# Performance work log

Hardware: AMD Instinct MI355X
Metric: run time of the kernel (lower is better)

The kernel has to match this reference:

```python
import jax, jax.numpy as jnp
import numpy as np
from jax import lax

CS = 64  # c_star


def _conv(x, w, pad, dil=1, groups=1):
    return lax.conv_general_dilated(
        x, w, (1, 1), ((pad[0], pad[0]), (pad[1], pad[1])),
        rhs_dilation=(dil, dil), dimension_numbers=('NCHW', 'OIHW', 'NCHW'),
        feature_group_count=groups)


def _bn(x, p, eps=1e-5):
    # p: [4, C] = (gamma, beta, running_mean, running_var), eval-mode batchnorm
    g, b, m, v = p
    s = g * lax.rsqrt(v + eps)
    return x * s[None, :, None, None] + (b - m * s)[None, :, None, None]


def _grid_sample(im, grid):
    # bilinear, padding_mode='zeros', align_corners=True
    # im: [B,C,H,W], grid: [B,H,W,2] with (x, y) in [-1, 1]
    B, C, H, W = im.shape
    gx = (grid[..., 0] + 1.0) * 0.5 * (W - 1)
    gy = (grid[..., 1] + 1.0) * 0.5 * (H - 1)
    x0 = jnp.floor(gx)
    y0 = jnp.floor(gy)
    wx = gx - x0
    wy = gy - y0

    def corner(ix, iy, w):
        valid = (ix >= 0) & (ix <= W - 1) & (iy >= 0) & (iy <= H - 1)
        ixc = jnp.clip(ix, 0, W - 1).astype(jnp.int32)
        iyc = jnp.clip(iy, 0, H - 1).astype(jnp.int32)
        vals = jax.vmap(lambda a, yy, xx: a[:, yy, xx])(im, iyc, ixc)  # [B,C,H,W]
        return vals * (w * valid)[:, None]

    return (corner(x0, y0, (1 - wx) * (1 - wy)) + corner(x0 + 1, y0, wx * (1 - wy))
            + corner(x0, y0 + 1, (1 - wx) * wy) + corner(x0 + 1, y0 + 1, wx * wy))


def _forward(x, w_reduce, bn_reduce, dcn_off_w, dcn_off_b, dcn_dw_w, dcn_pw_w, bn_dcn,
             w_d2, bn_d2, w_d3, bn_d3, w_asym1, bn_asym1, w_asym2, bn_asym2,
             ctx_weight, bn_star, eca_w, sp_w, blend_weight, w_expand, bn_expand):
    silu = jax.nn.silu
    h = silu(_bn(_conv(x, w_reduce, (0, 0)), bn_reduce))
    hs, hb = h[:, :CS], h[:, CS:]
    B, _, H, W = hs.shape
    # --- LightweightDCNv2 ---
    om = _conv(hs, dcn_off_w, (1, 1)) + dcn_off_b[None, :, None, None]
    off_y, off_x = om[:, 0], om[:, 1]
    mask = jax.nn.sigmoid(om[:, 2:3])
    gy, gx = jnp.meshgrid(jnp.linspace(-1.0, 1.0, H), jnp.linspace(-1.0, 1.0, W), indexing='ij')
    grid = jnp.stack([gx[None] + off_x * (2.0 / W), gy[None] + off_y * (2.0 / H)], axis=-1)
    xd = _grid_sample(hs, grid) * mask
    dcn = silu(_bn(_conv(_conv(xd, dcn_dw_w, (1, 1), groups=CS), dcn_pw_w, (0, 0)), bn_dcn))
    # --- context branches (depthwise dilated + asymmetric) ---
    d2 = silu(_bn(_conv(hs, w_d2, (2, 2), dil=2, groups=CS), bn_d2))
    d3 = silu(_bn(_conv(hs, w_d3, (3, 3), dil=3, groups=CS), bn_d3))
    a1 = silu(_bn(_conv(hs, w_asym1, (0, 3), groups=CS), bn_asym1))
    asym = silu(_bn(_conv(a1, w_asym2, (3, 0), groups=CS), bn_asym2))
    wv = jax.nn.softmax(ctx_weight)
    ctx = wv[0] * d2 + wv[1] * d3 + wv[2] * asym
    star = _bn(dcn * ctx, bn_star)
    # --- DualAttentionGate ---
    ych = star.mean((2, 3))[:, None, :]  # [B,1,C]
    ych = lax.conv_general_dilated(ych, eca_w, (1,), ((2, 2),),
                                   dimension_numbers=('NCH', 'OIH', 'NCH'))
    ych = jax.nn.sigmoid(ych).reshape(B, CS, 1, 1)
    star = star * ych
    sp = jnp.concatenate([star.mean(1, keepdims=True), star.max(1, keepdims=True)], axis=1)
    star = star * jax.nn.sigmoid(_conv(sp, sp_w, (3, 3)))
    # --- blend + shuffle + expand + residual ---
    alpha = jax.nn.sigmoid(blend_weight)
    out = jnp.concatenate([star * alpha, hb * (1.0 - alpha)], axis=1)
    c = out.shape[1]
    out = out.reshape(B, 2, c // 2, H, W).transpose(0, 2, 1, 3, 4).reshape(B, c, H, W)
    out = silu(_bn(_conv(out, w_expand, (0, 0)), bn_expand))
    return out + x


def setup_inputs() -> dict:
    ks = iter(jax.random.split(jax.random.key(0), 64))

    def nrm(shape, s=0.05):
        return jax.random.normal(next(ks), shape, jnp.float32) * s

    def bnp(C):
        return jnp.stack([1.0 + nrm((C,), 0.1), nrm((C,), 0.1), nrm((C,), 0.1),
                          0.5 + jax.random.uniform(next(ks), (C,), jnp.float32)])

    C1, C_, CSTAR = 256, 128, 64
    return dict(
        x=jax.random.normal(next(ks), (16, C1, 80, 80), jnp.float32),
        w_reduce=nrm((C_, C1, 1, 1)),
        bn_reduce=bnp(C_),
        dcn_off_w=nrm((3, CSTAR, 3, 3), 0.01),
        dcn_off_b=nrm((3,), 0.01),
        dcn_dw_w=nrm((CSTAR, 1, 3, 3), 0.2),
        dcn_pw_w=nrm((CSTAR, CSTAR, 1, 1), 0.1),
        bn_dcn=bnp(CSTAR),
        w_d2=nrm((CSTAR, 1, 3, 3), 0.2),
        bn_d2=bnp(CSTAR),
        w_d3=nrm((CSTAR, 1, 3, 3), 0.2),
        bn_d3=bnp(CSTAR),
        w_asym1=nrm((CSTAR, 1, 1, 7), 0.2),
        bn_asym1=bnp(CSTAR),
        w_asym2=nrm((CSTAR, 1, 7, 1), 0.2),
        bn_asym2=bnp(CSTAR),
        ctx_weight=jnp.ones(3, jnp.float32) / 3.0,
        bn_star=bnp(CSTAR),
        eca_w=nrm((1, 1, 5), 0.3),
        sp_w=nrm((1, 2, 7, 7), 0.1),
        blend_weight=jnp.asarray(0.5, jnp.float32),
        w_expand=nrm((C1, C_, 1, 1)),
        bn_expand=bnp(C1),
    )


def reference(x, w_reduce, bn_reduce, dcn_off_w, dcn_off_b, dcn_dw_w, dcn_pw_w, bn_dcn,
              w_d2, bn_d2, w_d3, bn_d3, w_asym1, bn_asym1, w_asym2, bn_asym2,
              ctx_weight, bn_star, eca_w, sp_w, blend_weight, w_expand, bn_expand):
    return _forward(x, w_reduce, bn_reduce, dcn_off_w, dcn_off_b, dcn_dw_w, dcn_pw_w, bn_dcn,
                    w_d2, bn_d2, w_d3, bn_d3, w_asym1, bn_asym1, w_asym2, bn_asym2,
                    ctx_weight, bn_star, eca_w, sp_w, blend_weight, w_expand, bn_expand)
```

## Files before the change

kernel.cpp:

```cpp
#include <hip/hip_runtime.h>

#define HH 80
#define WW 80
#define HWN 6400
#define BN 16

typedef unsigned short ushortT;
typedef __attribute__((ext_vector_type(8))) short short8;
typedef __attribute__((ext_vector_type(4))) float f32x4;

static constexpr size_t BIGN = (size_t)BN * 64 * HWN;

__device__ __forceinline__ float sigf(float v)  { return 1.f / (1.f + __expf(-v)); }
__device__ __forceinline__ float siluf(float v) { return v * sigf(v); }
__device__ __forceinline__ float tapf(const float* __restrict__ pl, int y, int x) {
  return ((unsigned)y < (unsigned)HH && (unsigned)x < (unsigned)WW) ? pl[y * WW + x] : 0.f;
}
__device__ __forceinline__ float bnap(float v, const float* __restrict__ bn, int c, int C) {
  float s = bn[c] * rsqrtf(bn[3 * C + c] + 1e-5f);
  return v * s + (bn[C + c] - bn[2 * C + c] * s);
}
__device__ __forceinline__ ushortT f2bf(float f) {
  unsigned u = __float_as_uint(f);
  return (ushortT)((u + 0x7FFFu + ((u >> 16) & 1u)) >> 16);
}
__device__ __forceinline__ void gl_lds16(const void* g, void* l) {
  __builtin_amdgcn_global_load_lds(
      (const __attribute__((address_space(1))) unsigned int*)g,
      (__attribute__((address_space(3))) unsigned int*)l, 16, 0, 0);
}
__device__ __forceinline__ int bs_w(int p, int k2) {
  return p * 20 + ((((k2 >> 2) ^ ((p >> 3) & 3)) << 2) | (k2 & 3));
}
__device__ __forceinline__ int bs_r(int p, int q) {
  return p * 20 + (((q ^ ((p >> 3) & 3)) << 2));
}

__global__ __launch_bounds__(256) void k_cvtw(const float* __restrict__ wr,
    const float* __restrict__ we, ushortT* __restrict__ wrb, ushortT* __restrict__ web) {
  int i = blockIdx.x * 256 + threadIdx.x;
  if (i < 32768) wrb[i] = f2bf(wr[i]);
  else           web[i - 32768] = f2bf(we[i - 32768]);
}

__global__ __launch_bounds__(256) void k_reduce_mfma(
    const float* __restrict__ x, const ushortT* __restrict__ Wb,
    const float* __restrict__ bn, float* __restrict__ hs, float* __restrict__ hb) {
  __shared__ ushortT As[128 * 32];
  __shared__ unsigned BsU[128 * 20];
  __shared__ float Ep[4 * 16 * 66];
  const int t = threadIdx.x;
  const int w = t >> 6, l = t & 63;
  const int p0 = blockIdx.x * 128;
  const int b = blockIdx.z;
  const int wm = (w >> 1) * 64, wn = (w & 1) * 64;
  f32x4 acc[4][4] = {};
  const float* xb = x + (size_t)b * 256 * HWN;
  const int srow = l >> 2, scol = (l & 3) * 8;
  for (int k0 = 0; k0 < 256; k0 += 32) {
    __syncthreads();
    gl_lds16(Wb + (size_t)((w * 2) * 16 + srow) * 256 + k0 + scol, &As[(w * 2) * 16 * 32]);
    gl_lds16(Wb + (size_t)((w * 2 + 1) * 16 + srow) * 256 + k0 + scol, &As[(w * 2 + 1) * 16 * 32]);
#pragma unroll
    for (int pass = 0; pass < 8; ++pass) {
      int idx = pass * 256 + t;
      int p_l = idx & 127, k2 = idx >> 7;
      int k = k0 + 2 * k2;
      float v0 = xb[(size_t)k * HWN + p0 + p_l];
      float v1 = xb[(size_t)(k + 1) * HWN + p0 + p_l];
      BsU[bs_w(p_l, k2)] = (unsigned)f2bf(v0) | ((unsigned)f2bf(v1) << 16);
    }
    __syncthreads();
    const int q = l >> 4, r16 = l & 15;
    short8 a[4], bv[4];
#pragma unroll
    for (int i = 0; i < 4; ++i)
      a[i] = *reinterpret_cast<const short8*>(&As[(wm + i * 16 + r16) * 32 + q * 8]);
#pragma unroll
    for (int j = 0; j < 4; ++j) {
      int row = wn + j * 16 + r16;
      bv[j] = *reinterpret_cast<const short8*>(&BsU[bs_r(row, q)]);
    }
#pragma unroll
    for (int i = 0; i < 4; ++i)
#pragma unroll
      for (int j = 0; j < 4; ++j)
        acc[i][j] = __builtin_amdgcn_mfma_f32_16x16x32_bf16(a[i], bv[j], acc[i][j], 0, 0, 0);
  }
  float* T = Ep + w * (16 * 66);
  const int col = l & 15, rowq = (l >> 4) * 4;
#pragma unroll
  for (int i = 0; i < 4; ++i) {
#pragma unroll
    for (int r = 0; r < 4; ++r)
#pragma unroll
      for (int j = 0; j < 4; ++j)
        T[(rowq + r) * 66 + j * 16 + col] = acc[i][j][r];
#pragma unroll
    for (int pass = 0; pass < 4; ++pass) {
      int row_l = pass * 4 + (l >> 4);
      const float4 v = *reinterpret_cast<const float4*>(&T[row_l * 66 + col * 4]);
      int c = wm + i * 16 + row_l;
      float s = bn[c] * rsqrtf(bn[384 + c] + 1e-5f);
      float tt = bn[128 + c] - bn[256 + c] * s;
      float4 o;
      o.x = siluf(v.x * s + tt);
      o.y = siluf(v.y * s + tt);
      o.z = siluf(v.z * s + tt);
      o.w = siluf(v.w * s + tt);
      float* dst = (c < 64 ? hs : hb) + ((size_t)b * 64 + (c & 63)) * HWN + p0 + wn + col * 4;
      *reinterpret_cast<float4*>(dst) = o;
    }
  }
}

__global__ __launch_bounds__(256) void k_offset(const float* __restrict__ hs,
    const float* __restrict__ w, const float* __restrict__ bias,
    float* __restrict__ sx, float* __restrict__ sy, float* __restrict__ msk) {
  __shared__ float tile[18 * 18];
  const int t = threadIdx.x;
  const int b = blockIdx.z;
  const int x0 = blockIdx.x * 16, y0 = blockIdx.y * 16;
  const int lx = t & 15, ly = t >> 4;
  float a0 = 0.f, a1 = 0.f, a2 = 0.f;
  for (int c = 0; c < 64; ++c) {
    __syncthreads();
    for (int i = t; i < 18 * 18; i += 256) {
      int tyy = i / 18, txx = i - tyy * 18;
      int gy = y0 + tyy - 1, gx = x0 + txx - 1;
      tile[i] = ((unsigned)gy < (unsigned)HH && (unsigned)gx < (unsigned)WW)
                    ? hs[((size_t)b * 64 + c) * HWN + gy * WW + gx] : 0.f;
    }
    __syncthreads();
    const float* wc = w + c * 9;
#pragma unroll
    for (int dy = 0; dy < 3; ++dy)
#pragma unroll
      for (int dx = 0; dx < 3; ++dx) {
        float v = tile[(ly + dy) * 18 + lx + dx];
        a0 = fmaf(wc[dy * 3 + dx], v, a0);
        a1 = fmaf(wc[576 + dy * 3 + dx], v, a1);
        a2 = fmaf(wc[1152 + dy * 3 + dx], v, a2);
      }
  }
  a0 += bias[0];
  a1 += bias[1];
  a2 += bias[2];
  size_t o = (size_t)b * HWN + (y0 + ly) * WW + x0 + lx;
  const float sc = 79.f / 80.f;
  sx[o] = (float)(x0 + lx) + a1 * sc;
  sy[o] = (float)(y0 + ly) + a0 * sc;
  msk[o] = sigf(a2);
}

__global__ __launch_bounds__(256) void k_gsdw(const float* __restrict__ hs,
    const float* __restrict__ sx, const float* __restrict__ sy,
    const float* __restrict__ msk, const float* __restrict__ wdw,
    float* __restrict__ outp) {
  __shared__ float tile[18 * 18];
  const int t = threadIdx.x;
  const int c = blockIdx.y, b = blockIdx.z;
  const int tx0 = (blockIdx.x % 5) * 16, ty0 = (blockIdx.x / 5) * 16;
  const float* pl = hs + ((size_t)b * 64 + c) * HWN;
  for (int i = t; i < 324; i += 256) {
    int iy = i / 18, ix = i - iy * 18;
    int gy = ty0 + iy - 1, gx = tx0 + ix - 1;
    float v = 0.f;
    if ((unsigned)gy < (unsigned)HH && (unsigned)gx < (unsigned)WW) {
      size_t o = (size_t)b * HWN + gy * WW + gx;
      float gxs = sx[o], gys = sy[o], m = msk[o];
      float x0f = floorf(gxs), y0f = floorf(gys);
      float wx = gxs - x0f, wy = gys - y0f;
      int ix0 = (int)x0f, iy0 = (int)y0f;
      int ix1 = ix0 + 1, iy1 = iy0 + 1;
      float acc = 0.f;
      if ((unsigned)iy0 < (unsigned)HH && (unsigned)ix0 < (unsigned)WW) acc = fmaf(pl[iy0 * WW + ix0], (1.f - wx) * (1.f - wy), acc);
      if ((unsigned)iy0 < (unsigned)HH && (unsigned)ix1 < (unsigned)WW) acc = fmaf(pl[iy0 * WW + ix1], wx * (1.f - wy), acc);
      if ((unsigned)iy1 < (unsigned)HH && (unsigned)ix0 < (unsigned)WW) acc = fmaf(pl[iy1 * WW + ix0], (1.f - wx) * wy, acc);
      if ((unsigned)iy1 < (unsigned)HH && (unsigned)ix1 < (unsigned)WW) acc = fmaf(pl[iy1 * WW + ix1], wx * wy, acc);
      v = acc * m;
    }
    tile[i] = v;
  }
  __syncthreads();
  const int lx = t & 15, ly = t >> 4;
  const float* wc = wdw + c * 9;
  float acc = 0.f;
#pragma unroll
  for (int dy = 0; dy < 3; ++dy)
#pragma unroll
    for (int dx = 0; dx < 3; ++dx)
      acc = fmaf(wc[dy * 3 + dx], tile[(ly + dy) * 18 + lx + dx], acc);
  outp[((size_t)b * 64 + c) * HWN + (ty0 + ly) * WW + tx0 + lx] = acc;
}

__global__ __launch_bounds__(256) void k_pw(const float* __restrict__ in,
    const float* __restrict__ w, const float* __restrict__ bn, float* __restrict__ outp) {
  __shared__ __align__(16) float Wt[1024];
  __shared__ __align__(16) float Xt[1024];
  const int t = threadIdx.x;
  const int p0 = blockIdx.x * 64, b = blockIdx.z;
  const int tx = t & 15, ty = t >> 4;
  float acc[4][4] = {};
  for (int k0 = 0; k0 < 64; k0 += 16) {
    __syncthreads();
    int idx = t;
#pragma unroll
    for (int r = 0; r < 4; ++r) {
      int c_l = idx >> 4, k_l = idx & 15;
      Wt[k_l * 64 + c_l] = w[c_l * 64 + k0 + k_l];
      idx += 256;
    }
    idx = t;
#pragma unroll
    for (int r = 0; r < 4; ++r) {
      int k_l = idx >> 6, p_l = idx & 63;
      Xt[k_l * 64 + p_l] = in[((size_t)b * 64 + k0 + k_l) * HWN + p0 + p_l];
      idx += 256;
    }
    __syncthreads();
#pragma unroll
    for (int kk = 0; kk < 16; ++kk) {
      const float4 wv = *reinterpret_cast<const float4*>(Wt + kk * 64 + ty * 4);
      const float4 xv = *reinterpret_cast<const float4*>(Xt + kk * 64 + tx * 4);
      const float wa[4] = {wv.x, wv.y, wv.z, wv.w};
      const float xa[4] = {xv.x, xv.y, xv.z, xv.w};
#pragma unroll
      for (int i = 0; i < 4; ++i)
#pragma unroll
        for (int j = 0; j < 4; ++j) acc[i][j] = fmaf(wa[i], xa[j], acc[i][j]);
    }
  }
#pragma unroll
  for (int i = 0; i < 4; ++i) {
    int c = ty * 4 + i;
    float s = bn[c] * rsqrtf(bn[192 + c] + 1e-5f);
    float tt = bn[64 + c] - bn[128 + c] * s;
    float4 o;
    o.x = siluf(acc[i][0] * s + tt);
    o.y = siluf(acc[i][1] * s + tt);
    o.z = siluf(acc[i][2] * s + tt);
    o.w = siluf(acc[i][3] * s + tt);
    *reinterpret_cast<float4*>(outp + ((size_t)b * 64 + c) * HWN + p0 + tx * 4) = o;
  }
}

__global__ __launch_bounds__(256) void k_ctxstar(const float* __restrict__ hs,
    const float* __restrict__ dcn,
    const float* __restrict__ wd2, const float* __restrict__ bnd2,
    const float* __restrict__ wd3, const float* __restrict__ bnd3,
    const float* __restrict__ wa1, const float* __restrict__ bna1,
    const float* __restrict__ wa2, const float* __restrict__ bna2,
    const float* __restrict__ cw, const float* __restrict__ bnstar,
    float* __restrict__ star0) {
  __shared__ float ht[22 * 23];
  __shared__ float at[22 * 17];
  const int t = threadIdx.x;
  const int c = blockIdx.y, b = blockIdx.z;
  const int tx0 = (blockIdx.x % 5) * 16, ty0 = (blockIdx.x / 5) * 16;
  const float* pl = hs + ((size_t)b * 64 + c) * HWN;
  for (int i = t; i < 484; i += 256) {
    int iy = i / 22, ix = i - iy * 22;
    int gy = ty0 + iy - 3, gx = tx0 + ix - 3;
    ht[iy * 23 + ix] = ((unsigned)gy < (unsigned)HH && (unsigned)gx < (unsigned)WW)
                           ? pl[gy * WW + gx] : 0.f;
  }
  __syncthreads();
  for (int i = t; i < 352; i += 256) {
    int iy = i >> 4, ix = i & 15;
    int gy = ty0 + iy - 3;
    float v = 0.f;
    if ((unsigned)gy < (unsigned)HH) {
      float s = 0.f;
#pragma unroll
      for (int k = 0; k < 7; ++k) s = fmaf(wa1[c * 7 + k], ht[iy * 23 + ix + k], s);
      v = siluf(bnap(s, bna1, c, 64));
    }
    at[iy * 17 + ix] = v;
  }
  __syncthreads();
  const int lx = t & 15, ly = t >> 4;
  float d2 = 0.f, d3 = 0.f;
#pragma unroll
  for (int dy = 0; dy < 3; ++dy)
#pragma unroll
    for (int dx = 0; dx < 3; ++dx) {
      float w2 = wd2[c * 9 + dy * 3 + dx], w3 = wd3[c * 9 + dy * 3 + dx];
      d2 = fmaf(w2, ht[(ly + 3 + 2 * (dy - 1)) * 23 + lx + 3 + 2 * (dx - 1)], d2);
      d3 = fmaf(w3, ht[(ly + 3 + 3 * (dy - 1)) * 23 + lx + 3 + 3 * (dx - 1)], d3);
    }
  float as = 0.f;
#pragma unroll
  for (int k = 0; k < 7; ++k) as = fmaf(wa2[c * 7 + k], at[(ly + k) * 17 + lx], as);
  d2 = siluf(bnap(d2, bnd2, c, 64));
  d3 = siluf(bnap(d3, bnd3, c, 64));
  as = siluf(bnap(as, bna2, c, 64));
  float e0 = __expf(cw[0]), e1 = __expf(cw[1]), e2 = __expf(cw[2]);
  float inv = 1.f / (e0 + e1 + e2);
  float ctx = (e0 * d2 + e1 * d3 + e2 * as) * inv;
  size_t o = ((size_t)b * 64 + c) * HWN + (ty0 + ly) * WW + tx0 + lx;
  star0[o] = bnap(dcn[o] * ctx, bnstar, c, 64);
}

__global__ __launch_bounds__(256) void k_cmean(const float* __restrict__ star0,
    float* __restrict__ mean) {
  const int c = blockIdx.x, b = blockIdx.y;
  const float* pl = star0 + ((size_t)b * 64 + c) * HWN;
  float s = 0.f;
  for (int i = threadIdx.x; i < HWN; i += 256) s += pl[i];
  __shared__ float red[256];
  red[threadIdx.x] = s;
  __syncthreads();
  for (int st = 128; st > 0; st >>= 1) {
    if (threadIdx.x < st) red[threadIdx.x] += red[threadIdx.x + st];
    __syncthreads();
  }
  if (threadIdx.x == 0) mean[b * 64 + c] = red[0] * (1.f / HWN);
}

__global__ __launch_bounds__(1024) void k_eca(const float* __restrict__ mean,
    const float* __restrict__ ew, float* __restrict__ ych) {
  const int t = threadIdx.x;
  const int c = t & 63;
  const int base = t - c;
  float acc = 0.f;
#pragma unroll
  for (int k = 0; k < 5; ++k) {
    int cc = c + k - 2;
    if ((unsigned)cc < 64u) acc = fmaf(ew[k], mean[base + cc], acc);
  }
  ych[t] = sigf(acc);
}

__global__ __launch_bounds__(256) void k_spstats(const float* __restrict__ star0,
    const float* __restrict__ ych, float* __restrict__ spmean, float* __restrict__ spmax) {
  __shared__ float yc[64];
  if (threadIdx.x < 64) yc[threadIdx.x] = ych[blockIdx.y * 64 + threadIdx.x];
  __syncthreads();
  const int p = blockIdx.x * 256 + threadIdx.x;
  const int b = blockIdx.y;
  float s = 0.f, mx = -1e30f;
  for (int c = 0; c < 64; ++c) {
    float v = star0[((size_t)b * 64 + c) * HWN + p] * yc[c];
    s += v;
    mx = fmaxf(mx, v);
  }
  spmean[(size_t)b * HWN + p] = s * (1.f / 64.f);
  spmax[(size_t)b * HWN + p] = mx;
}

__global__ __launch_bounds__(256) void k_spconv(const float* __restrict__ spmean,
    const float* __restrict__ spmax, const float* __restrict__ w,
    float* __restrict__ spat) {
  const int p = blockIdx.x * 256 + threadIdx.x;
  const int b = blockIdx.y;
  const int y = p / WW, x = p - y * WW;
  const float* me = spmean + (size_t)b * HWN;
  const float* mx = spmax + (size_t)b * HWN;
  float acc = 0.f;
#pragma unroll
  for (int dy = 0; dy < 7; ++dy) {
    int yy = y + dy - 3;
    if ((unsigned)yy >= (unsigned)HH) continue;
#pragma unroll
    for (int dx = 0; dx < 7; ++dx) {
      int xx = x + dx - 3;
      if ((unsigned)xx >= (unsigned)WW) continue;
      acc = fmaf(w[dy * 7 + dx], me[yy * WW + xx], acc);
      acc = fmaf(w[49 + dy * 7 + dx], mx[yy * WW + xx], acc);
    }
  }
  spat[(size_t)b * HWN + p] = sigf(acc);
}

__global__ __launch_bounds__(256) void k_expand_mfma(
    const float* __restrict__ star0, const float* __restrict__ hbuf,
    const float* __restrict__ ych, const float* __restrict__ spat,
    const float* __restrict__ blend, const ushortT* __restrict__ Wb,
    const float* __restrict__ bn, const float* __restrict__ xin,
    float* __restrict__ outp) {
  __shared__ ushortT As[128 * 32];
  __shared__ unsigned BsU[128 * 20];
  __shared__ float Ep[4 * 16 * 66];
  __shared__ float Sp[128];
  __shared__ float Yc[64];
  const int t = threadIdx.x;
  const int w = t >> 6, l = t & 63;
  const int p0 = blockIdx.x * 128;
  const int c0 = blockIdx.y * 128;
  const int b = blockIdx.z;
  const int wm = (w >> 1) * 64, wn = (w & 1) * 64;
  const float alpha = sigf(blend[0]);
  const float beta = 1.f - alpha;
  if (t < 128) Sp[t] = alpha * spat[(size_t)b * HWN + p0 + t];
  else if (t < 192) Yc[t - 128] = ych[b * 64 + (t - 128)];
  f32x4 acc[4][4] = {};
  const int srow = l >> 2, scol = (l & 3) * 8;
  for (int k0 = 0; k0 < 128; k0 += 32) {
    __syncthreads();
    gl_lds16(Wb + (size_t)(c0 + (w * 2) * 16 + srow) * 128 + k0 + scol, &As[(w * 2) * 16 * 32]);
    gl_lds16(Wb + (size_t)(c0 + (w * 2 + 1) * 16 + srow) * 128 + k0 + scol, &As[(w * 2 + 1) * 16 * 32]);
    const int ch0 = k0 >> 1;
#pragma unroll
    for (int pass = 0; pass < 8; ++pass) {
      int idx = pass * 256 + t;
      int p_l = idx & 127, chl = idx >> 7;
      int ch = ch0 + chl;
      size_t o = ((size_t)b * 64 + ch) * HWN + p0 + p_l;
      float vs = star0[o] * Yc[ch] * Sp[p_l];
      float vh = beta * hbuf[o];
      BsU[bs_w(p_l, chl)] = (unsigned)f2bf(vs) | ((unsigned)f2bf(vh) << 16);
    }
    __syncthreads();
    const int q = l >> 4, r16 = l & 15;
    short8 a[4], bv[4];
#pragma unroll
    for (int i = 0; i < 4; ++i)
      a[i] = *reinterpret_cast<const short8*>(&As[(wm + i * 16 + r16) * 32 + q * 8]);
#pragma unroll
    for (int j = 0; j < 4; ++j) {
      int row = wn + j * 16 + r16;
      bv[j] = *reinterpret_cast<const short8*>(&BsU[bs_r(row, q)]);
    }
#pragma unroll
    for (int i = 0; i < 4; ++i)
#pragma unroll
      for (int j = 0; j < 4; ++j)
        acc[i][j] = __builtin_amdgcn_mfma_f32_16x16x32_bf16(a[i], bv[j], acc[i][j], 0, 0, 0);
  }
  float* T = Ep + w * (16 * 66);
  const int col = l & 15, rowq = (l >> 4) * 4;
#pragma unroll
  for (int i = 0; i < 4; ++i) {
#pragma unroll
    for (int r = 0; r < 4; ++r)
#pragma unroll
      for (int j = 0; j < 4; ++j)
        T[(rowq + r) * 66 + j * 16 + col] = acc[i][j][r];
#pragma unroll
    for (int pass = 0; pass < 4; ++pass) {
      int row_l = pass * 4 + (l >> 4);
      const float4 v = *reinterpret_cast<const float4*>(&T[row_l * 66 + col * 4]);
      int c = c0 + wm + i * 16 + row_l;
      float s = bn[c] * rsqrtf(bn[768 + c] + 1e-5f);
      float tt = bn[256 + c] - bn[512 + c] * s;
      size_t o = ((size_t)b * 256 + c) * HWN + p0 + wn + col * 4;
      const float4 xr = *reinterpret_cast<const float4*>(xin + o);
      float4 ov;
      ov.x = siluf(v.x * s + tt) + xr.x;
      ov.y = siluf(v.y * s + tt) + xr.y;
      ov.z = siluf(v.z * s + tt) + xr.z;
      ov.w = siluf(v.w * s + tt) + xr.w;
      *reinterpret_cast<float4*>(outp + o) = ov;
    }
  }
}

extern "C" void kernel_launch(void* const* d_in, const int* in_sizes, int n_in,
                              void* d_out, int out_size, void* d_ws, size_t ws_size,
                              hipStream_t stream) {
  const float* x         = (const float*)d_in[0];
  const float* w_reduce  = (const float*)d_in[1];
  const float* bn_reduce = (const float*)d_in[2];
  const float* dcn_off_w = (const float*)d_in[3];
  const float* dcn_off_b = (const float*)d_in[4];
  const float* dcn_dw_w  = (const float*)d_in[5];
  const float* dcn_pw_w  = (const float*)d_in[6];
  const float* bn_dcn    = (const float*)d_in[7];
  const float* w_d2      = (const float*)d_in[8];
  const float* bn_d2     = (const float*)d_in[9];
  const float* w_d3      = (const float*)d_in[10];
  const float* bn_d3     = (const float*)d_in[11];
  const float* w_asym1   = (const float*)d_in[12];
  const float* bn_asym1  = (const float*)d_in[13];
  const float* w_asym2   = (const float*)d_in[14];
  const float* bn_asym2  = (const float*)d_in[15];
  const float* ctx_w     = (const float*)d_in[16];
  const float* bn_star   = (const float*)d_in[17];
  const float* eca_w     = (const float*)d_in[18];
  const float* sp_w      = (const float*)d_in[19];
  const float* blend     = (const float*)d_in[20];
  const float* w_expand  = (const float*)d_in[21];
  const float* bn_expand = (const float*)d_in[22];
  float* out = (float*)d_out;
  float* ws = (float*)d_ws;

  float* slotA = ws;
  float* slotB = ws + BIGN;
  float* slotC = ws + 2 * BIGN;
  float* slotD = ws + 3 * BIGN;
  float* sm = ws + 4 * BIGN;
  float* sx     = sm;
  float* sy     = sm + 102400;
  float* msk    = sm + 204800;
  float* spmean = sx;
  float* spmax  = sy;
  float* spat   = msk;
  float* cmean  = sm + 307200;
  float* ych    = sm + 308224;
  ushortT* Wrb = (ushortT*)(sm + 309248);
  ushortT* Web = Wrb + 32768;

  k_cvtw<<<dim3(256), 256, 0, stream>>>(w_reduce, w_expand, Wrb, Web);
  k_reduce_mfma<<<dim3(50, 1, 16), 256, 0, stream>>>(x, Wrb, bn_reduce, slotA, slotB);
  k_offset<<<dim3(5, 5, 16), 256, 0, stream>>>(slotA, dcn_off_w, dcn_off_b, sx, sy, msk);
  k_gsdw<<<dim3(25, 64, 16), 256, 0, stream>>>(slotA, sx, sy, msk, dcn_dw_w, slotC);
  k_pw<<<dim3(100, 1, 16), 256, 0, stream>>>(slotC, dcn_pw_w, bn_dcn, slotD);
  k_ctxstar<<<dim3(25, 64, 16), 256, 0, stream>>>(slotA, slotD, w_d2, bn_d2,
                                                  w_d3, bn_d3, w_asym1, bn_asym1,
                                                  w_asym2, bn_asym2, ctx_w, bn_star, slotD);
  k_cmean<<<dim3(64, 16), 256, 0, stream>>>(slotD, cmean);
  k_eca<<<dim3(1), 1024, 0, stream>>>(cmean, eca_w, ych);
  k_spstats<<<dim3(25, 16), 256, 0, stream>>>(slotD, ych, spmean, spmax);
  k_spconv<<<dim3(25, 16), 256, 0, stream>>>(spmean, spmax, sp_w, spat);
  k_expand_mfma<<<dim3(50, 2, 16), 256, 0, stream>>>(slotD, slotB, ych, spat, blend,
                                                     Web, bn_expand, x, out);
}
```

Baseline: 518.3 us.

## Port pointwise conv to bf16 MFMA and retune offset, spstats, epilogue padding

```diff
diff --git a/kernel.cpp b/kernel.cpp
--- a/kernel.cpp
+++ b/kernel.cpp
@@ -13,9 +13,6 @@
 
 __device__ __forceinline__ float sigf(float v)  { return 1.f / (1.f + __expf(-v)); }
 __device__ __forceinline__ float siluf(float v) { return v * sigf(v); }
-__device__ __forceinline__ float tapf(const float* __restrict__ pl, int y, int x) {
-  return ((unsigned)y < (unsigned)HH && (unsigned)x < (unsigned)WW) ? pl[y * WW + x] : 0.f;
-}
 __device__ __forceinline__ float bnap(float v, const float* __restrict__ bn, int c, int C) {
   float s = bn[c] * rsqrtf(bn[3 * C + c] + 1e-5f);
   return v * s + (bn[C + c] - bn[2 * C + c] * s);
@@ -37,10 +34,12 @@
 }
 
 __global__ __launch_bounds__(256) void k_cvtw(const float* __restrict__ wr,
-    const float* __restrict__ we, ushortT* __restrict__ wrb, ushortT* __restrict__ web) {
+    const float* __restrict__ we, const float* __restrict__ wp,
+    ushortT* __restrict__ wrb, ushortT* __restrict__ web, ushortT* __restrict__ wpb) {
   int i = blockIdx.x * 256 + threadIdx.x;
   if (i < 32768) wrb[i] = f2bf(wr[i]);
-  else           web[i - 32768] = f2bf(we[i - 32768]);
+  else if (i < 65536) web[i - 32768] = f2bf(we[i - 32768]);
+  else if (i < 69632) wpb[i - 65536] = f2bf(wp[i - 65536]);
 }
 
 __global__ __launch_bounds__(256) void k_reduce_mfma(
@@ -48,7 +47,7 @@
     const float* __restrict__ bn, float* __restrict__ hs, float* __restrict__ hb) {
   __shared__ ushortT As[128 * 32];
   __shared__ unsigned BsU[128 * 20];
-  __shared__ float Ep[4 * 16 * 66];
+  __shared__ float Ep[4 * 16 * 68];
   const int t = threadIdx.x;
   const int w = t >> 6, l = t & 63;
   const int p0 = blockIdx.x * 128;
@@ -87,7 +86,7 @@
       for (int j = 0; j < 4; ++j)
         acc[i][j] = __builtin_amdgcn_mfma_f32_16x16x32_bf16(a[i], bv[j], acc[i][j], 0, 0, 0);
   }
-  float* T = Ep + w * (16 * 66);
+  float* T = Ep + w * (16 * 68);
   const int col = l & 15, rowq = (l >> 4) * 4;
 #pragma unroll
   for (int i = 0; i < 4; ++i) {
@@ -95,11 +94,11 @@
     for (int r = 0; r < 4; ++r)
 #pragma unroll
       for (int j = 0; j < 4; ++j)
-        T[(rowq + r) * 66 + j * 16 + col] = acc[i][j][r];
+        T[(rowq + r) * 68 + j * 16 + col] = acc[i][j][r];
 #pragma unroll
     for (int pass = 0; pass < 4; ++pass) {
       int row_l = pass * 4 + (l >> 4);
-      const float4 v = *reinterpret_cast<const float4*>(&T[row_l * 66 + col * 4]);
+      const float4 v = *reinterpret_cast<const float4*>(&T[row_l * 68 + col * 4]);
       int c = wm + i * 16 + row_l;
       float s = bn[c] * rsqrtf(bn[384 + c] + 1e-5f);
       float tt = bn[128 + c] - bn[256 + c] * s;
@@ -117,31 +116,37 @@
 __global__ __launch_bounds__(256) void k_offset(const float* __restrict__ hs,
     const float* __restrict__ w, const float* __restrict__ bias,
     float* __restrict__ sx, float* __restrict__ sy, float* __restrict__ msk) {
-  __shared__ float tile[18 * 18];
-  const int t = threadIdx.x;
-  const int b = blockIdx.z;
-  const int x0 = blockIdx.x * 16, y0 = blockIdx.y * 16;
+  __shared__ float ht[16 * 324];
+  __shared__ float wt[1728];
+  const int t = threadIdx.x;
+  const int b = blockIdx.y;
+  const int x0 = (blockIdx.x % 5) * 16, y0 = (blockIdx.x / 5) * 16;
   const int lx = t & 15, ly = t >> 4;
+  for (int i = t; i < 1728; i += 256) wt[i] = w[i];
   float a0 = 0.f, a1 = 0.f, a2 = 0.f;
-  for (int c = 0; c < 64; ++c) {
-    __syncthreads();
-    for (int i = t; i < 18 * 18; i += 256) {
-      int tyy = i / 18, txx = i - tyy * 18;
-      int gy = y0 + tyy - 1, gx = x0 + txx - 1;
-      tile[i] = ((unsigned)gy < (unsigned)HH && (unsigned)gx < (unsigned)WW)
-                    ? hs[((size_t)b * 64 + c) * HWN + gy * WW + gx] : 0.f;
-    }
-    __syncthreads();
-    const float* wc = w + c * 9;
-#pragma unroll
-    for (int dy = 0; dy < 3; ++dy)
-#pragma unroll
-      for (int dx = 0; dx < 3; ++dx) {
-        float v = tile[(ly + dy) * 18 + lx + dx];
-        a0 = fmaf(wc[dy * 3 + dx], v, a0);
-        a1 = fmaf(wc[576 + dy * 3 + dx], v, a1);
-        a2 = fmaf(wc[1152 + dy * 3 + dx], v, a2);
-      }
+  for (int r = 0; r < 4; ++r) {
+    __syncthreads();
+    for (int i = t; i < 16 * 324; i += 256) {
+      int ch = i / 324, pos = i - ch * 324;
+      int iy = pos / 18, ix = pos - iy * 18;
+      int gy = y0 + iy - 1, gx = x0 + ix - 1;
+      ht[i] = ((unsigned)gy < (unsigned)HH && (unsigned)gx < (unsigned)WW)
+                  ? hs[((size_t)b * 64 + r * 16 + ch) * HWN + gy * WW + gx] : 0.f;
+    }
+    __syncthreads();
+    for (int ch = 0; ch < 16; ++ch) {
+      const float* base = &ht[ch * 324];
+      const int c = r * 16 + ch;
+#pragma unroll
+      for (int dy = 0; dy < 3; ++dy)
+#pragma unroll
+        for (int dx = 0; dx < 3; ++dx) {
+          float v = base[(ly + dy) * 18 + lx + dx];
+          a0 = fmaf(wt[c * 9 + dy * 3 + dx], v, a0);
+          a1 = fmaf(wt[576 + c * 9 + dy * 3 + dx], v, a1);
+          a2 = fmaf(wt[1152 + c * 9 + dy * 3 + dx], v, a2);
+        }
+    }
   }
   a0 += bias[0];
   a1 += bias[1];
@@ -194,54 +199,72 @@
   outp[((size_t)b * 64 + c) * HWN + (ty0 + ly) * WW + tx0 + lx] = acc;
 }
 
-__global__ __launch_bounds__(256) void k_pw(const float* __restrict__ in,
-    const float* __restrict__ w, const float* __restrict__ bn, float* __restrict__ outp) {
-  __shared__ __align__(16) float Wt[1024];
-  __shared__ __align__(16) float Xt[1024];
-  const int t = threadIdx.x;
-  const int p0 = blockIdx.x * 64, b = blockIdx.z;
-  const int tx = t & 15, ty = t >> 4;
-  float acc[4][4] = {};
-  for (int k0 = 0; k0 < 64; k0 += 16) {
-    __syncthreads();
-    int idx = t;
-#pragma unroll
-    for (int r = 0; r < 4; ++r) {
-      int c_l = idx >> 4, k_l = idx & 15;
-      Wt[k_l * 64 + c_l] = w[c_l * 64 + k0 + k_l];
-      idx += 256;
-    }
-    idx = t;
-#pragma unroll
-    for (int r = 0; r < 4; ++r) {
-      int k_l = idx >> 6, p_l = idx & 63;
-      Xt[k_l * 64 + p_l] = in[((size_t)b * 64 + k0 + k_l) * HWN + p0 + p_l];
-      idx += 256;
-    }
-    __syncthreads();
-#pragma unroll
-    for (int kk = 0; kk < 16; ++kk) {
-      const float4 wv = *reinterpret_cast<const float4*>(Wt + kk * 64 + ty * 4);
-      const float4 xv = *reinterpret_cast<const float4*>(Xt + kk * 64 + tx * 4);
-      const float wa[4] = {wv.x, wv.y, wv.z, wv.w};
-      const float xa[4] = {xv.x, xv.y, xv.z, xv.w};
-#pragma unroll
-      for (int i = 0; i < 4; ++i)
-#pragma unroll
-        for (int j = 0; j < 4; ++j) acc[i][j] = fmaf(wa[i], xa[j], acc[i][j]);
-    }
-  }
+__global__ __launch_bounds__(256) void k_pw_mfma(const float* __restrict__ in,
+    const ushortT* __restrict__ Wpb, const float* __restrict__ bn,
+    float* __restrict__ outp) {
+  __shared__ ushortT As[2][64 * 32];
+  __shared__ unsigned BsU[128 * 20];
+  __shared__ float Ep[4 * 16 * 36];
+  const int t = threadIdx.x;
+  const int w = t >> 6, l = t & 63;
+  const int p0 = blockIdx.x * 128;
+  const int b = blockIdx.y;
+  const int wn = w * 32;
+  f32x4 acc[4][2] = {};
+  const int srow = l >> 2, scol = (l & 3) * 8;
+  gl_lds16(Wpb + (size_t)(w * 16 + srow) * 64 + scol,      &As[0][w * 16 * 32]);
+  gl_lds16(Wpb + (size_t)(w * 16 + srow) * 64 + 32 + scol, &As[1][w * 16 * 32]);
+  for (int kc = 0; kc < 2; ++kc) {
+    __syncthreads();
+    const int ch0 = kc * 32;
+#pragma unroll
+    for (int pass = 0; pass < 8; ++pass) {
+      int idx = pass * 256 + t;
+      int p_l = idx & 127, k2 = idx >> 7;
+      int k = ch0 + 2 * k2;
+      float v0 = in[((size_t)b * 64 + k) * HWN + p0 + p_l];
+      float v1 = in[((size_t)b * 64 + k + 1) * HWN + p0 + p_l];
+      BsU[bs_w(p_l, k2)] = (unsigned)f2bf(v0) | ((unsigned)f2bf(v1) << 16);
+    }
+    __syncthreads();
+    const int q = l >> 4, r16 = l & 15;
+    short8 a[4], bv[2];
+#pragma unroll
+    for (int i = 0; i < 4; ++i)
+      a[i] = *reinterpret_cast<const short8*>(&As[kc][(i * 16 + r16) * 32 + q * 8]);
+#pragma unroll
+    for (int j = 0; j < 2; ++j)
+      bv[j] = *reinterpret_cast<const short8*>(&BsU[bs_r(wn + j * 16 + r16, q)]);
+#pragma unroll
+    for (int i = 0; i < 4; ++i)
+#pragma unroll
+      for (int j = 0; j < 2; ++j)
+        acc[i][j] = __builtin_amdgcn_mfma_f32_16x16x32_bf16(a[i], bv[j], acc[i][j], 0, 0, 0);
+  }
+  float* T = Ep + w * (16 * 36);
+  const int col = l & 15, rowq = (l >> 4) * 4;
 #pragma unroll
   for (int i = 0; i < 4; ++i) {
-    int c = ty * 4 + i;
-    float s = bn[c] * rsqrtf(bn[192 + c] + 1e-5f);
-    float tt = bn[64 + c] - bn[128 + c] * s;
-    float4 o;
-    o.x = siluf(acc[i][0] * s + tt);
-    o.y = siluf(acc[i][1] * s + tt);
-    o.z = siluf(acc[i][2] * s + tt);
-    o.w = siluf(acc[i][3] * s + tt);
-    *reinterpret_cast<float4*>(outp + ((size_t)b * 64 + c) * HWN + p0 + tx * 4) = o;
+#pragma unroll
+    for (int r = 0; r < 4; ++r)
+#pragma unroll
+      for (int j = 0; j < 2; ++j)
+        T[(rowq + r) * 36 + j * 16 + col] = acc[i][j][r];
+#pragma unroll
+    for (int pass = 0; pass < 2; ++pass) {
+      int flat = pass * 64 + l;
+      int row_l = flat >> 3, c4 = flat & 7;
+      const float4 v = *reinterpret_cast<const float4*>(&T[row_l * 36 + c4 * 4]);
+      int c = i * 16 + row_l;
+      float s = bn[c] * rsqrtf(bn[192 + c] + 1e-5f);
+      float tt = bn[64 + c] - bn[128 + c] * s;
+      float4 o;
+      o.x = siluf(v.x * s + tt);
+      o.y = siluf(v.y * s + tt);
+      o.z = siluf(v.z * s + tt);
+      o.w = siluf(v.w * s + tt);
+      *reinterpret_cast<float4*>(outp + ((size_t)b * 64 + c) * HWN + p0 + wn + c4 * 4) = o;
+    }
   }
 }
 
@@ -335,18 +358,29 @@
 __global__ __launch_bounds__(256) void k_spstats(const float* __restrict__ star0,
     const float* __restrict__ ych, float* __restrict__ spmean, float* __restrict__ spmax) {
   __shared__ float yc[64];
-  if (threadIdx.x < 64) yc[threadIdx.x] = ych[blockIdx.y * 64 + threadIdx.x];
+  __shared__ float rs[4][64], rm[4][64];
+  const int t = threadIdx.x;
+  const int b = blockIdx.y;
+  const int p0 = blockIdx.x * 64;
+  if (t < 64) yc[t] = ych[b * 64 + t];
   __syncthreads();
-  const int p = blockIdx.x * 256 + threadIdx.x;
-  const int b = blockIdx.y;
+  const int tq = t >> 6, pix = t & 63;
   float s = 0.f, mx = -1e30f;
-  for (int c = 0; c < 64; ++c) {
-    float v = star0[((size_t)b * 64 + c) * HWN + p] * yc[c];
+  for (int cc = 0; cc < 16; ++cc) {
+    int c = tq * 16 + cc;
+    float v = star0[((size_t)b * 64 + c) * HWN + p0 + pix] * yc[c];
     s += v;
     mx = fmaxf(mx, v);
   }
-  spmean[(size_t)b * HWN + p] = s * (1.f / 64.f);
-  spmax[(size_t)b * HWN + p] = mx;
+  rs[tq][pix] = s;
+  rm[tq][pix] = mx;
+  __syncthreads();
+  if (t < 64) {
+    float ss = rs[0][t] + rs[1][t] + rs[2][t] + rs[3][t];
+    float mm = fmaxf(fmaxf(rm[0][t], rm[1][t]), fmaxf(rm[2][t], rm[3][t]));
+    spmean[(size_t)b * HWN + p0 + t] = ss * (1.f / 64.f);
+    spmax[(size_t)b * HWN + p0 + t] = mm;
+  }
 }
 
 __global__ __launch_bounds__(256) void k_spconv(const float* __restrict__ spmean,
@@ -381,7 +415,7 @@
     float* __restrict__ outp) {
   __shared__ ushortT As[128 * 32];
   __shared__ unsigned BsU[128 * 20];
-  __shared__ float Ep[4 * 16 * 66];
+  __shared__ float Ep[4 * 16 * 68];
   __shared__ float Sp[128];
   __shared__ float Yc[64];
   const int t = threadIdx.x;
@@ -428,7 +462,7 @@
       for (int j = 0; j < 4; ++j)
         acc[i][j] = __builtin_amdgcn_mfma_f32_16x16x32_bf16(a[i], bv[j], acc[i][j], 0, 0, 0);
   }
-  float* T = Ep + w * (16 * 66);
+  float* T = Ep + w * (16 * 68);
   const int col = l & 15, rowq = (l >> 4) * 4;
 #pragma unroll
   for (int i = 0; i < 4; ++i) {
@@ -436,11 +470,11 @@
     for (int r = 0; r < 4; ++r)
 #pragma unroll
       for (int j = 0; j < 4; ++j)
-        T[(rowq + r) * 66 + j * 16 + col] = acc[i][j][r];
+        T[(rowq + r) * 68 + j * 16 + col] = acc[i][j][r];
 #pragma unroll
     for (int pass = 0; pass < 4; ++pass) {
       int row_l = pass * 4 + (l >> 4);
-      const float4 v = *reinterpret_cast<const float4*>(&T[row_l * 66 + col * 4]);
+      const float4 v = *reinterpret_cast<const float4*>(&T[row_l * 68 + col * 4]);
       int c = c0 + wm + i * 16 + row_l;
       float s = bn[c] * rsqrtf(bn[768 + c] + 1e-5f);
       float tt = bn[256 + c] - bn[512 + c] * s;
@@ -500,18 +534,19 @@
   float* ych    = sm + 308224;
   ushortT* Wrb = (ushortT*)(sm + 309248);
   ushortT* Web = Wrb + 32768;
-
-  k_cvtw<<<dim3(256), 256, 0, stream>>>(w_reduce, w_expand, Wrb, Web);
+  ushortT* Wpb = Web + 32768;
+
+  k_cvtw<<<dim3(272), 256, 0, stream>>>(w_reduce, w_expand, dcn_pw_w, Wrb, Web, Wpb);
   k_reduce_mfma<<<dim3(50, 1, 16), 256, 0, stream>>>(x, Wrb, bn_reduce, slotA, slotB);
-  k_offset<<<dim3(5, 5, 16), 256, 0, stream>>>(slotA, dcn_off_w, dcn_off_b, sx, sy, msk);
+  k_offset<<<dim3(25, 16), 256, 0, stream>>>(slotA, dcn_off_w, dcn_off_b, sx, sy, msk);
   k_gsdw<<<dim3(25, 64, 16), 256, 0, stream>>>(slotA, sx, sy, msk, dcn_dw_w, slotC);
-  k_pw<<<dim3(100, 1, 16), 256, 0, stream>>>(slotC, dcn_pw_w, bn_dcn, slotD);
+  k_pw_mfma<<<dim3(50, 16), 256, 0, stream>>>(slotC, Wpb, bn_dcn, slotD);
   k_ctxstar<<<dim3(25, 64, 16), 256, 0, stream>>>(slotA, slotD, w_d2, bn_d2,
                                                   w_d3, bn_d3, w_asym1, bn_asym1,
                                                   w_asym2, bn_asym2, ctx_w, bn_star, slotD);
   k_cmean<<<dim3(64, 16), 256, 0, stream>>>(slotD, cmean);
   k_eca<<<dim3(1), 1024, 0, stream>>>(cmean, eca_w, ych);
-  k_spstats<<<dim3(25, 16), 256, 0, stream>>>(slotD, ych, spmean, spmax);
+  k_spstats<<<dim3(100, 16), 256, 0, stream>>>(slotD, ych, spmean, spmax);
   k_spconv<<<dim3(25, 16), 256, 0, stream>>>(spmean, spmax, sp_w, spat);
   k_expand_mfma<<<dim3(50, 2, 16), 256, 0, stream>>>(slotD, slotB, ych, spat, blend,
                                                      Web, bn_expand, x, out);
```

Result: faster. 478.1 us (-7.8%).
